# Kernel optimization log

Hardware: AMD Instinct MI355X
Metric: run time of the kernel (lower is better)

Reference implementation:

```python
import jax, jax.numpy as jnp
import numpy as np

N_E = 8192
E_DIM = 256
BETA = 0.25

def setup_inputs() -> dict:
    key = jax.random.key(0)
    k1, k2 = jax.random.split(key)
    z = jax.random.normal(k1, (2, 16384, E_DIM), dtype=jnp.float32)
    # matches nn.Embedding init: uniform(-1/n_e, 1/n_e)
    emb = jax.random.uniform(k2, (N_E, E_DIM), minval=-1.0 / N_E, maxval=1.0 / N_E, dtype=jnp.float32)
    code_age = jnp.zeros((N_E,), jnp.float32)
    code_usage = jnp.zeros((N_E,), jnp.float32)
    return {"z": z, "emb": emb, "code_age": code_age, "code_usage": code_usage}

def reference(z, emb, code_age, code_usage):
    sg = jax.lax.stop_gradient
    zf = z.reshape(-1, emb.shape[1])  # [M, D]
    # squared euclidean distances; argmin is identical to torch.cdist argmin
    d = (jnp.sum(zf * zf, axis=1, keepdims=True)
         - 2.0 * (zf @ emb.T)
         + jnp.sum(emb * emb, axis=1)[None, :])  # [M, n_e]
    idx = jnp.argmin(d, axis=1)  # [M]
    z_q = emb[idx].reshape(z.shape)
    loss = BETA * jnp.mean((sg(z_q) - z) ** 2) + jnp.mean((z_q - sg(z)) ** 2)
    z_q_st = z + sg(z_q - z)  # straight-through
    # code stats: age reset for used codes, usage histogram via scatter-add
    new_code_age = (code_age + 1.0).at[idx].set(0.0)
    new_code_usage = code_usage.at[idx].add(jnp.ones_like(idx, dtype=code_usage.dtype))
    return z_q_st, loss, idx, new_code_age, new_code_usage
```

## Files before the change

kernel.cpp:

```cpp
#include <hip/hip_runtime.h>
#include <math.h>

#define D_DIM 256
#define NE    8192
#define M_TOT 32768L

#define O_LOSS  8388608L
#define O_IDX   8388609L
#define O_AGE   8421377L
#define O_USAGE 8429569L

typedef __attribute__((ext_vector_type(8))) short bf16x8;
typedef __attribute__((ext_vector_type(4))) short bf16x4;
typedef __attribute__((ext_vector_type(4))) float f32x4;

__device__ __forceinline__ short f2bf(float f) {
  unsigned u = __float_as_uint(f);
  u += 0x7FFFu + ((u >> 16) & 1u);
  return (short)(u >> 16);
}
__device__ __forceinline__ float bf2f(short s) {
  return __uint_as_float(((unsigned)(unsigned short)s) << 16);
}

__global__ __launch_bounds__(256) void vq_prep(
    const float* __restrict__ z, const float* __restrict__ emb,
    const float* __restrict__ code_age, const float* __restrict__ code_usage,
    float* __restrict__ out, float* __restrict__ zzf, float* __restrict__ enf,
    int* __restrict__ cnt) {
  int t = blockIdx.x * 256 + threadIdx.x;
  {
    const float4* row = reinterpret_cast<const float4*>(z + (size_t)t * D_DIM);
    double s = 0.0;
#pragma unroll
    for (int q = 0; q < D_DIM / 4; ++q) {
      float4 v = row[q];
      s = fma((double)v.x, (double)v.x, s);
      s = fma((double)v.y, (double)v.y, s);
      s = fma((double)v.z, (double)v.z, s);
      s = fma((double)v.w, (double)v.w, s);
    }
    zzf[t] = (float)s;
  }
  if (t < NE) {
    const float4* row = reinterpret_cast<const float4*>(emb + (size_t)t * D_DIM);
    double s = 0.0;
#pragma unroll
    for (int q = 0; q < D_DIM / 4; ++q) {
      float4 v = row[q];
      s = fma((double)v.x, (double)v.x, s);
      s = fma((double)v.y, (double)v.y, s);
      s = fma((double)v.z, (double)v.z, s);
      s = fma((double)v.w, (double)v.w, s);
    }
    enf[t] = (float)s;
    out[O_AGE + t] = code_age[t] + 1.0f;
    out[O_USAGE + t] = code_usage[t];
    if (t == 0) { out[O_LOSS] = 0.0f; *cnt = 0; }
  }
}

__global__ __launch_bounds__(256) void vq_split(
    const float* __restrict__ emb, short* __restrict__ emb_h,
    short* __restrict__ emb_l) {
  int e4 = blockIdx.x * 256 + threadIdx.x;
  float4 v = reinterpret_cast<const float4*>(emb)[e4];
  float s[4] = {v.x, v.y, v.z, v.w};
  short h[4], l[4];
#pragma unroll
  for (int i = 0; i < 4; ++i) {
    h[i] = f2bf(s[i]);
    l[i] = f2bf(s[i] - bf2f(h[i]));
  }
  *reinterpret_cast<bf16x4*>(emb_h + (size_t)e4 * 4) = (bf16x4){h[0], h[1], h[2], h[3]};
  *reinterpret_cast<bf16x4*>(emb_l + (size_t)e4 * 4) = (bf16x4){l[0], l[1], l[2], l[3]};
}

#define LDK 40
#define LSLICE (128 * LDK)
#define CHUNK 4096
#define MSPLIT 4

template <int PRESPLIT>
__global__ __launch_bounds__(512, 2) void vq_argmin_mfma(
    const float* __restrict__ z, const float* __restrict__ emb,
    const short* __restrict__ emb_h, const short* __restrict__ emb_l,
    const float* __restrict__ zzf, const float* __restrict__ enf,
    float* __restrict__ pv1, float* __restrict__ pv2, int* __restrict__ pj1) {
  __shared__ short th[2][LSLICE];
  __shared__ short tl[2][LSLICE];

  const int tid = threadIdx.x;
  const int lane = tid & 63;
  const int wave = tid >> 6;
  const int wr = wave >> 1;
  const int wc = wave & 1;
  const int lrow = lane & 15;
  const int lq = lane >> 4;
  const size_t row0 = (size_t)blockIdx.x * 128;
  const int jbase = blockIdx.y * CHUNK;

  const int srow = tid >> 2;
  const int skq = (tid & 3) * 8;

  bf16x8 afh[2][8], afl[2][8];
#pragma unroll
  for (int ks = 0; ks < 8; ++ks) {
    __syncthreads();
    {
      const float* src = z + (row0 + srow) * (size_t)D_DIM + ks * 32 + skq;
      float4 v0 = *reinterpret_cast<const float4*>(src);
      float4 v1 = *reinterpret_cast<const float4*>(src + 4);
      float s[8] = {v0.x, v0.y, v0.z, v0.w, v1.x, v1.y, v1.z, v1.w};
      short h[8], l[8];
#pragma unroll
      for (int i = 0; i < 8; ++i) {
        h[i] = f2bf(s[i]);
        l[i] = f2bf(s[i] - bf2f(h[i]));
      }
      *reinterpret_cast<bf16x4*>(&th[0][srow * LDK + skq]) = (bf16x4){h[0], h[1], h[2], h[3]};
      *reinterpret_cast<bf16x4*>(&th[0][srow * LDK + skq + 4]) = (bf16x4){h[4], h[5], h[6], h[7]};
      *reinterpret_cast<bf16x4*>(&tl[0][srow * LDK + skq]) = (bf16x4){l[0], l[1], l[2], l[3]};
      *reinterpret_cast<bf16x4*>(&tl[0][srow * LDK + skq + 4]) = (bf16x4){l[4], l[5], l[6], l[7]};
    }
    __syncthreads();
#pragma unroll
    for (int rt = 0; rt < 2; ++rt) {
      int r = wr * 32 + rt * 16 + lrow;
      afh[rt][ks] = *reinterpret_cast<const bf16x8*>(&th[0][r * LDK + lq * 8]);
      afl[rt][ks] = *reinterpret_cast<const bf16x8*>(&tl[0][r * LDK + lq * 8]);
    }
  }

  float zrow2[8];
#pragma unroll
  for (int rt = 0; rt < 2; ++rt)
#pragma unroll
    for (int rr = 0; rr < 4; ++rr)
      zrow2[rt * 4 + rr] = zzf[row0 + wr * 32 + rt * 16 + lq * 4 + rr];

  float bv1[8], bv2[8];
  int bj1[8];
#pragma unroll
  for (int s = 0; s < 8; ++s) { bv1[s] = INFINITY; bv2[s] = INFINITY; bj1[s] = 0; }

  bf16x8 ph, pl;
  float4 pf0, pf1;

  if (PRESPLIT) {
    ph = *reinterpret_cast<const bf16x8*>(emb_h + (size_t)(jbase + srow) * D_DIM + skq);
    pl = *reinterpret_cast<const bf16x8*>(emb_l + (size_t)(jbase + srow) * D_DIM + skq);
  } else {
    const float* src = emb + (size_t)(jbase + srow) * D_DIM + skq;
    pf0 = *reinterpret_cast<const float4*>(src);
    pf1 = *reinterpret_cast<const float4*>(src + 4);
  }
  __syncthreads();
  if (PRESPLIT) {
    *reinterpret_cast<bf16x8*>(&th[0][srow * LDK + skq]) = ph;
    *reinterpret_cast<bf16x8*>(&tl[0][srow * LDK + skq]) = pl;
    ph = *reinterpret_cast<const bf16x8*>(emb_h + (size_t)(jbase + srow) * D_DIM + 32 + skq);
    pl = *reinterpret_cast<const bf16x8*>(emb_l + (size_t)(jbase + srow) * D_DIM + 32 + skq);
  } else {
    float s[8] = {pf0.x, pf0.y, pf0.z, pf0.w, pf1.x, pf1.y, pf1.z, pf1.w};
    short h[8], l[8];
#pragma unroll
    for (int i = 0; i < 8; ++i) {
      h[i] = f2bf(s[i]);
      l[i] = f2bf(s[i] - bf2f(h[i]));
    }
    *reinterpret_cast<bf16x4*>(&th[0][srow * LDK + skq]) = (bf16x4){h[0], h[1], h[2], h[3]};
    *reinterpret_cast<bf16x4*>(&th[0][srow * LDK + skq + 4]) = (bf16x4){h[4], h[5], h[6], h[7]};
    *reinterpret_cast<bf16x4*>(&tl[0][srow * LDK + skq]) = (bf16x4){l[0], l[1], l[2], l[3]};
    *reinterpret_cast<bf16x4*>(&tl[0][srow * LDK + skq + 4]) = (bf16x4){l[4], l[5], l[6], l[7]};
    const float* src = emb + (size_t)(jbase + srow) * D_DIM + 32 + skq;
    pf0 = *reinterpret_cast<const float4*>(src);
    pf1 = *reinterpret_cast<const float4*>(src + 4);
  }
  asm volatile("s_waitcnt lgkmcnt(0)" ::: "memory");
  __builtin_amdgcn_s_barrier();
  asm volatile("" ::: "memory");

  for (int jt0 = jbase; jt0 < jbase + CHUNK; jt0 += 128) {
    float enq[4];
#pragma unroll
    for (int ct = 0; ct < 4; ++ct) enq[ct] = enf[jt0 + wc * 64 + ct * 16 + lrow];

    f32x4 acc[2][4];
#pragma unroll
    for (int rt = 0; rt < 2; ++rt)
#pragma unroll
      for (int ct = 0; ct < 4; ++ct) acc[rt][ct] = (f32x4){0.f, 0.f, 0.f, 0.f};

#pragma unroll
    for (int ks = 0; ks < 8; ++ks) {
      const int p = ks & 1;
      bf16x8 bfh[4];
#pragma unroll
      for (int ct = 0; ct < 4; ++ct) {
        int c = wc * 64 + ct * 16 + lrow;
        bfh[ct] = *reinterpret_cast<const bf16x8*>(&th[p][c * LDK + lq * 8]);
      }
      __builtin_amdgcn_s_setprio(1);
#pragma unroll
      for (int rt = 0; rt < 2; ++rt)
#pragma unroll
        for (int ct = 0; ct < 4; ++ct) {
          acc[rt][ct] = __builtin_amdgcn_mfma_f32_16x16x32_bf16(
              afl[rt][ks], bfh[ct], acc[rt][ct], 0, 0, 0);
          acc[rt][ct] = __builtin_amdgcn_mfma_f32_16x16x32_bf16(
              afh[rt][ks], bfh[ct], acc[rt][ct], 0, 0, 0);
        }
      __builtin_amdgcn_s_setprio(0);

      if (PRESPLIT) {
        *reinterpret_cast<bf16x8*>(&th[p ^ 1][srow * LDK + skq]) = ph;
        *reinterpret_cast<bf16x8*>(&tl[p ^ 1][srow * LDK + skq]) = pl;
      } else {
        float s[8] = {pf0.x, pf0.y, pf0.z, pf0.w, pf1.x, pf1.y, pf1.z, pf1.w};
        short h[8], l[8];
#pragma unroll
        for (int i = 0; i < 8; ++i) {
          h[i] = f2bf(s[i]);
          l[i] = f2bf(s[i] - bf2f(h[i]));
        }
        *reinterpret_cast<bf16x4*>(&th[p ^ 1][srow * LDK + skq]) = (bf16x4){h[0], h[1], h[2], h[3]};
        *reinterpret_cast<bf16x4*>(&th[p ^ 1][srow * LDK + skq + 4]) = (bf16x4){h[4], h[5], h[6], h[7]};
        *reinterpret_cast<bf16x4*>(&tl[p ^ 1][srow * LDK + skq]) = (bf16x4){l[0], l[1], l[2], l[3]};
        *reinterpret_cast<bf16x4*>(&tl[p ^ 1][srow * LDK + skq + 4]) = (bf16x4){l[4], l[5], l[6], l[7]};
      }
      {
        int sl = ((jt0 - jbase) >> 4) + ks + 2;
        if (sl > CHUNK / 16 - 1) sl = CHUNK / 16 - 1;
        const size_t off = ((size_t)(jbase + (sl >> 3) * 128 + srow)) * D_DIM
                         + (sl & 7) * 32 + skq;
        if (PRESPLIT) {
          ph = *reinterpret_cast<const bf16x8*>(emb_h + off);
          pl = *reinterpret_cast<const bf16x8*>(emb_l + off);
        } else {
          pf0 = *reinterpret_cast<const float4*>(emb + off);
          pf1 = *reinterpret_cast<const float4*>(emb + off + 4);
        }
      }

      bf16x8 bfl[4];
#pragma unroll
      for (int ct = 0; ct < 4; ++ct) {
        int c = wc * 64 + ct * 16 + lrow;
        bfl[ct] = *reinterpret_cast<const bf16x8*>(&tl[p][c * LDK + lq * 8]);
      }
      __builtin_amdgcn_s_setprio(1);
#pragma unroll
      for (int rt = 0; rt < 2; ++rt)
#pragma unroll
        for (int ct = 0; ct < 4; ++ct)
          acc[rt][ct] = __builtin_amdgcn_mfma_f32_16x16x32_bf16(
              afh[rt][ks], bfl[ct], acc[rt][ct], 0, 0, 0);
      __builtin_amdgcn_s_setprio(0);

      asm volatile("s_waitcnt lgkmcnt(0)" ::: "memory");
      __builtin_amdgcn_s_barrier();
      asm volatile("" ::: "memory");
    }

#pragma unroll
    for (int ct = 0; ct < 4; ++ct) {
      int gj = jt0 + wc * 64 + ct * 16 + lrow;
      float ef = enq[ct];
#pragma unroll
      for (int rt = 0; rt < 2; ++rt)
#pragma unroll
        for (int rr = 0; rr < 4; ++rr) {
          int s = rt * 4 + rr;
          float t = zrow2[s] - 2.0f * acc[rt][ct][rr];
          float dv = t + ef;
          bj1[s] = (dv < bv1[s]) ? gj : bj1[s];
          bv2[s] = fminf(bv2[s], fmaxf(dv, bv1[s]));
          bv1[s] = fminf(bv1[s], dv);
        }
    }
  }

#pragma unroll
  for (int m = 1; m < 16; m <<= 1) {
#pragma unroll
    for (int s = 0; s < 8; ++s) {
      float ov1 = __shfl_xor(bv1[s], m, 16);
      float ov2 = __shfl_xor(bv2[s], m, 16);
      int oj1 = __shfl_xor(bj1[s], m, 16);
      if (ov1 < bv1[s] || (ov1 == bv1[s] && oj1 < bj1[s])) {
        bv2[s] = fminf(bv1[s], ov2);
        bv1[s] = ov1; bj1[s] = oj1;
      } else {
        bv2[s] = fminf(bv2[s], ov1);
      }
    }
  }
  if (lrow == 0) {
#pragma unroll
    for (int s = 0; s < 8; ++s) {
      size_t grow = row0 + wr * 32 + (s >> 2) * 16 + lq * 4 + (s & 3);
      size_t o = (size_t)(blockIdx.y * 2 + wc) * M_TOT + grow;
      pv1[o] = bv1[s]; pv2[o] = bv2[s]; pj1[o] = bj1[s];
    }
  }
}

__global__ __launch_bounds__(256) void vq_merge(
    const float* __restrict__ pv1, const float* __restrict__ pv2,
    const int* __restrict__ pj1, int* __restrict__ idx_ws,
    int* __restrict__ cnt, int* __restrict__ flagged,
    float* __restrict__ flagv1, int* __restrict__ gnc) {
  int m = blockIdx.x * 256 + threadIdx.x;
  if (m >= M_TOT) return;
  float v1 = INFINITY, v2 = INFINITY;
  int j1 = 0;
#pragma unroll
  for (int s = 0; s < MSPLIT; ++s) {
    float a1 = pv1[(size_t)s * M_TOT + m];
    float a2 = pv2[(size_t)s * M_TOT + m];
    int aj = pj1[(size_t)s * M_TOT + m];
    if (a1 < v1 || (a1 == v1 && aj < j1)) {
      v2 = fminf(v1, a2); v1 = a1; j1 = aj;
    } else {
      v2 = fminf(v2, a1);
    }
  }
  idx_ws[m] = j1;
  float u = ldexpf(1.0f, ilogbf(v2) - 23);
  if (v2 - v1 <= 2.0f * u + 1e-5f) {
    int p = atomicAdd(cnt, 1);
    flagged[p] = m;
    flagv1[p] = v1;
    gnc[p] = 0;
  }
}

#define RSPLIT 8
#define RCHUNK (NE / RSPLIT)
#define GCAP 16

template <int PRESPLIT>
__global__ __launch_bounds__(512, 2) void vq_refine_scan(
    const float* __restrict__ z, const float* __restrict__ emb,
    const short* __restrict__ emb_h, const short* __restrict__ emb_l,
    const float* __restrict__ zzf, const float* __restrict__ enf,
    const int* __restrict__ cnt, const int* __restrict__ flagged,
    const float* __restrict__ flagv1, int* __restrict__ gnc,
    int* __restrict__ gcj) {
  int n = *cnt;
  if (n > (int)M_TOT) n = (int)M_TOT;
  const int base = blockIdx.x * 128;
  if (base >= n) return;

  __shared__ short th[2][LSLICE];
  __shared__ short tl[2][LSLICE];
  __shared__ int rowm_s[128];
  __shared__ float thr_s[128];
  __shared__ float rzz_s[128];

  const int tid = threadIdx.x;
  const int lane = tid & 63;
  const int wave = tid >> 6;
  const int wr = wave >> 1;
  const int wc = wave & 1;
  const int lrow = lane & 15;
  const int lq = lane >> 4;
  const int cb = blockIdx.y * RCHUNK;

  const int srow = tid >> 2;
  const int skq = (tid & 3) * 8;

  if (tid < 128) {
    bool valid = (base + tid) < n;
    int m = valid ? flagged[base + tid] : flagged[base];
    rowm_s[tid] = m;
    rzz_s[tid] = zzf[m];
    if (valid) {
      float v1 = flagv1[base + tid];
      float u = ldexpf(1.0f, ilogbf(v1) - 23);
      thr_s[tid] = v1 + 4.0f * u + 2.5e-5f;
    } else {
      thr_s[tid] = -INFINITY;
    }
  }

  bf16x8 afh[2][8], afl[2][8];
#pragma unroll
  for (int ks = 0; ks < 8; ++ks) {
    __syncthreads();
    {
      const float* src = z + (size_t)rowm_s[srow] * D_DIM + ks * 32 + skq;
      float4 v0 = *reinterpret_cast<const float4*>(src);
      float4 v1 = *reinterpret_cast<const float4*>(src + 4);
      float s[8] = {v0.x, v0.y, v0.z, v0.w, v1.x, v1.y, v1.z, v1.w};
      short h[8], l[8];
#pragma unroll
      for (int i = 0; i < 8; ++i) {
        h[i] = f2bf(s[i]);
        l[i] = f2bf(s[i] - bf2f(h[i]));
      }
      *reinterpret_cast<bf16x4*>(&th[0][srow * LDK + skq]) = (bf16x4){h[0], h[1], h[2], h[3]};
      *reinterpret_cast<bf16x4*>(&th[0][srow * LDK + skq + 4]) = (bf16x4){h[4], h[5], h[6], h[7]};
      *reinterpret_cast<bf16x4*>(&tl[0][srow * LDK + skq]) = (bf16x4){l[0], l[1], l[2], l[3]};
      *reinterpret_cast<bf16x4*>(&tl[0][srow * LDK + skq + 4]) = (bf16x4){l[4], l[5], l[6], l[7]};
    }
    __syncthreads();
#pragma unroll
    for (int rt = 0; rt < 2; ++rt) {
      int r = wr * 32 + rt * 16 + lrow;
      afh[rt][ks] = *reinterpret_cast<const bf16x8*>(&th[0][r * LDK + lq * 8]);
      afl[rt][ks] = *reinterpret_cast<const bf16x8*>(&tl[0][r * LDK + lq * 8]);
    }
  }

  float zrow2[8], thr8[8];
  int rcix8[8];
#pragma unroll
  for (int rt = 0; rt < 2; ++rt)
#pragma unroll
    for (int rr = 0; rr < 4; ++rr) {
      int s = rt * 4 + rr;
      int lrloc = wr * 32 + rt * 16 + lq * 4 + rr;
      zrow2[s] = rzz_s[lrloc];
      thr8[s] = thr_s[lrloc];
      rcix8[s] = base + lrloc;
    }

  bf16x8 ph, pl;
  float4 pf0, pf1;

  if (PRESPLIT) {
    ph = *reinterpret_cast<const bf16x8*>(emb_h + (size_t)(cb + srow) * D_DIM + skq);
    pl = *reinterpret_cast<const bf16x8*>(emb_l + (size_t)(cb + srow) * D_DIM + skq);
  } else {
    const float* src = emb + (size_t)(cb + srow) * D_DIM + skq;
    pf0 = *reinterpret_cast<const float4*>(src);
    pf1 = *reinterpret_cast<const float4*>(src + 4);
  }
  __syncthreads();
  if (PRESPLIT) {
    *reinterpret_cast<bf16x8*>(&th[0][srow * LDK + skq]) = ph;
    *reinterpret_cast<bf16x8*>(&tl[0][srow * LDK + skq]) = pl;
    ph = *reinterpret_cast<const bf16x8*>(emb_h + (size_t)(cb + srow) * D_DIM + 32 + skq);
    pl = *reinterpret_cast<const bf16x8*>(emb_l + (size_t)(cb + srow) * D_DIM + 32 + skq);
  } else {
    float s[8] = {pf0.x, pf0.y, pf0.z, pf0.w, pf1.x, pf1.y, pf1.z, pf1.w};
    short h[8], l[8];
#pragma unroll
    for (int i = 0; i < 8; ++i) {
      h[i] = f2bf(s[i]);
      l[i] = f2bf(s[i] - bf2f(h[i]));
    }
    *reinterpret_cast<bf16x4*>(&th[0][srow * LDK + skq]) = (bf16x4){h[0], h[1], h[2], h[3]};
    *reinterpret_cast<bf16x4*>(&th[0][srow * LDK + skq + 4]) = (bf16x4){h[4], h[5], h[6], h[7]};
    *reinterpret_cast<bf16x4*>(&tl[0][srow * LDK + skq]) = (bf16x4){l[0], l[1], l[2], l[3]};
    *reinterpret_cast<bf16x4*>(&tl[0][srow * LDK + skq + 4]) = (bf16x4){l[4], l[5], l[6], l[7]};
    const float* src = emb + (size_t)(cb + srow) * D_DIM + 32 + skq;
    pf0 = *reinterpret_cast<const float4*>(src);
    pf1 = *reinterpret_cast<const float4*>(src + 4);
  }
  asm volatile("s_waitcnt lgkmcnt(0)" ::: "memory");
  __builtin_amdgcn_s_barrier();
  asm volatile("" ::: "memory");

  for (int jt0 = cb; jt0 < cb + RCHUNK; jt0 += 128) {
    float enq[4];
#pragma unroll
    for (int ct = 0; ct < 4; ++ct) enq[ct] = enf[jt0 + wc * 64 + ct * 16 + lrow];

    f32x4 acc[2][4];
#pragma unroll
    for (int rt = 0; rt < 2; ++rt)
#pragma unroll
      for (int ct = 0; ct < 4; ++ct) acc[rt][ct] = (f32x4){0.f, 0.f, 0.f, 0.f};

#pragma unroll
    for (int ks = 0; ks < 8; ++ks) {
      const int p = ks & 1;
      bf16x8 bfh[4];
#pragma unroll
      for (int ct = 0; ct < 4; ++ct) {
        int c = wc * 64 + ct * 16 + lrow;
        bfh[ct] = *reinterpret_cast<const bf16x8*>(&th[p][c * LDK + lq * 8]);
      }
      __builtin_amdgcn_s_setprio(1);
#pragma unroll
      for (int rt = 0; rt < 2; ++rt)
#pragma unroll
        for (int ct = 0; ct < 4; ++ct) {
          acc[rt][ct] = __builtin_amdgcn_mfma_f32_16x16x32_bf16(
              afl[rt][ks], bfh[ct], acc[rt][ct], 0, 0, 0);
          acc[rt][ct] = __builtin_amdgcn_mfma_f32_16x16x32_bf16(
              afh[rt][ks], bfh[ct], acc[rt][ct], 0, 0, 0);
        }
      __builtin_amdgcn_s_setprio(0);

      if (PRESPLIT) {
        *reinterpret_cast<bf16x8*>(&th[p ^ 1][srow * LDK + skq]) = ph;
        *reinterpret_cast<bf16x8*>(&tl[p ^ 1][srow * LDK + skq]) = pl;
      } else {
        float s[8] = {pf0.x, pf0.y, pf0.z, pf0.w, pf1.x, pf1.y, pf1.z, pf1.w};
        short h[8], l[8];
#pragma unroll
        for (int i = 0; i < 8; ++i) {
          h[i] = f2bf(s[i]);
          l[i] = f2bf(s[i] - bf2f(h[i]));
        }
        *reinterpret_cast<bf16x4*>(&th[p ^ 1][srow * LDK + skq]) = (bf16x4){h[0], h[1], h[2], h[3]};
        *reinterpret_cast<bf16x4*>(&th[p ^ 1][srow * LDK + skq + 4]) = (bf16x4){h[4], h[5], h[6], h[7]};
        *reinterpret_cast<bf16x4*>(&tl[p ^ 1][srow * LDK + skq]) = (bf16x4){l[0], l[1], l[2], l[3]};
        *reinterpret_cast<bf16x4*>(&tl[p ^ 1][srow * LDK + skq + 4]) = (bf16x4){l[4], l[5], l[6], l[7]};
      }
      {
        int sl = ((jt0 - cb) >> 4) + ks + 2;
        if (sl > RCHUNK / 16 - 1) sl = RCHUNK / 16 - 1;
        const size_t off = ((size_t)(cb + (sl >> 3) * 128 + srow)) * D_DIM
                         + (sl & 7) * 32 + skq;
        if (PRESPLIT) {
          ph = *reinterpret_cast<const bf16x8*>(emb_h + off);
          pl = *reinterpret_cast<const bf16x8*>(emb_l + off);
        } else {
          pf0 = *reinterpret_cast<const float4*>(emb + off);
          pf1 = *reinterpret_cast<const float4*>(emb + off + 4);
        }
      }

      bf16x8 bfl[4];
#pragma unroll
      for (int ct = 0; ct < 4; ++ct) {
        int c = wc * 64 + ct * 16 + lrow;
        bfl[ct] = *reinterpret_cast<const bf16x8*>(&tl[p][c * LDK + lq * 8]);
      }
      __builtin_amdgcn_s_setprio(1);
#pragma unroll
      for (int rt = 0; rt < 2; ++rt)
#pragma unroll
        for (int ct = 0; ct < 4; ++ct)
          acc[rt][ct] = __builtin_amdgcn_mfma_f32_16x16x32_bf16(
              afh[rt][ks], bfl[ct], acc[rt][ct], 0, 0, 0);
      __builtin_amdgcn_s_setprio(0);

      asm volatile("s_waitcnt lgkmcnt(0)" ::: "memory");
      __builtin_amdgcn_s_barrier();
      asm volatile("" ::: "memory");
    }

#pragma unroll
    for (int ct = 0; ct < 4; ++ct) {
      int gj = jt0 + wc * 64 + ct * 16 + lrow;
      float ef = enq[ct];
#pragma unroll
      for (int rt = 0; rt < 2; ++rt)
#pragma unroll
        for (int rr = 0; rr < 4; ++rr) {
          int s = rt * 4 + rr;
          float t = zrow2[s] - 2.0f * acc[rt][ct][rr];
          float dv = t + ef;
          if (dv <= thr8[s]) {
            int p = atomicAdd(&gnc[rcix8[s]], 1);
            if (p < GCAP) gcj[rcix8[s] * GCAP + p] = gj;
          }
        }
    }
  }
}

__global__ __launch_bounds__(256) void vq_refine_fin(
    const float* __restrict__ z, const float* __restrict__ emb,
    const float* __restrict__ zzf, const float* __restrict__ enf,
    int* __restrict__ idx_ws, const int* __restrict__ cnt,
    const int* __restrict__ flagged, const int* __restrict__ gnc,
    const int* __restrict__ gcj) {
  __shared__ float zs[D_DIM];
  __shared__ float cdv[GCAP];
  __shared__ float rv[256];
  __shared__ int rj[256];

  const int tid = threadIdx.x;
  int n = *cnt;
  if (n > (int)M_TOT) n = (int)M_TOT;

  for (int rc = blockIdx.x; rc < n; rc += gridDim.x) {
    int m = flagged[rc];
    __syncthreads();
    zs[tid] = z[(size_t)m * D_DIM + tid];
    __syncthreads();
    int nc = gnc[rc];
    float rzz = zzf[m];

    if (nc >= 1 && nc <= GCAP) {
      if (tid < nc) {
        int j = gcj[rc * GCAP + tid];
        const float4* er = reinterpret_cast<const float4*>(emb + (size_t)j * D_DIM);
        double a = 0.0;
#pragma unroll 4
        for (int k4 = 0; k4 < D_DIM / 4; ++k4) {
          float4 ev = er[k4];
          float4 zv = *reinterpret_cast<const float4*>(&zs[k4 * 4]);
          a = fma((double)zv.x, (double)ev.x, a);
          a = fma((double)zv.y, (double)ev.y, a);
          a = fma((double)zv.z, (double)ev.z, a);
          a = fma((double)zv.w, (double)ev.w, a);
        }
        float zef = (float)a;
        float t = rzz - 2.0f * zef;
        cdv[tid] = t + enf[j];
      }
      __syncthreads();
      if (tid == 0) {
        float bvv = INFINITY; int bjj = 0x7FFFFFFF;
        for (int c = 0; c < nc; ++c) {
          float dv = cdv[c]; int j = gcj[rc * GCAP + c];
          if (dv < bvv || (dv == bvv && j < bjj)) { bvv = dv; bjj = j; }
        }
        idx_ws[m] = bjj;
      }
    } else if (nc > GCAP) {
      float bvv = INFINITY; int bjj = 0;
      for (int j = tid; j < NE; j += 256) {
        const float4* er = reinterpret_cast<const float4*>(emb + (size_t)j * D_DIM);
        double a = 0.0;
        for (int k4 = 0; k4 < D_DIM / 4; ++k4) {
          float4 ev = er[k4];
          float4 zv = *reinterpret_cast<const float4*>(&zs[k4 * 4]);
          a = fma((double)zv.x, (double)ev.x, a);
          a = fma((double)zv.y, (double)ev.y, a);
          a = fma((double)zv.z, (double)ev.z, a);
          a = fma((double)zv.w, (double)ev.w, a);
        }
        float zef = (float)a;
        float t = rzz - 2.0f * zef;
        float dv = t + enf[j];
        if (dv < bvv) { bvv = dv; bjj = j; }
      }
      rv[tid] = bvv; rj[tid] = bjj;
      __syncthreads();
      for (int s = 128; s > 0; s >>= 1) {
        if (tid < s) {
          float ov = rv[tid + s]; int oj = rj[tid + s];
          if (ov < rv[tid] || (ov == rv[tid] && oj < rj[tid])) {
            rv[tid] = ov; rj[tid] = oj;
          }
        }
        __syncthreads();
      }
      if (tid == 0) idx_ws[m] = rj[0];
    }
  }
}

__global__ __launch_bounds__(256) void vq_scatter(
    const int* __restrict__ idx_ws, float* __restrict__ out) {
  int m = blockIdx.x * 256 + threadIdx.x;
  if (m >= M_TOT) return;
  int j = idx_ws[m];
  out[O_IDX + m] = (float)j;
  out[O_AGE + j] = 0.0f;
  atomicAdd(&out[O_USAGE + j], 1.0f);
}

__global__ __launch_bounds__(256) void vq_gather(
    const float* __restrict__ z, const float* __restrict__ emb,
    const int* __restrict__ idx_ws, float* __restrict__ out) {
  __shared__ float lsum[4];
  size_t e4 = (size_t)blockIdx.x * 256 + threadIdx.x;
  size_t m = e4 >> 6;
  int dq = (int)(e4 & 63);
  int j = idx_ws[m];
  float4 q = *reinterpret_cast<const float4*>(emb + (size_t)j * D_DIM + dq * 4);
  float4 zv = *reinterpret_cast<const float4*>(z + e4 * 4);
  float dx = q.x - zv.x, dy = q.y - zv.y, dz = q.z - zv.z, dw = q.w - zv.w;
  float4 o;
  o.x = zv.x + dx; o.y = zv.y + dy; o.z = zv.z + dz; o.w = zv.w + dw;
  *reinterpret_cast<float4*>(out + e4 * 4) = o;
  float ls = dx * dx + dy * dy + dz * dz + dw * dw;
#pragma unroll
  for (int off = 32; off > 0; off >>= 1) ls += __shfl_down(ls, off, 64);
  if ((threadIdx.x & 63) == 0) lsum[threadIdx.x >> 6] = ls;
  __syncthreads();
  if (threadIdx.x == 0)
    atomicAdd(out + O_LOSS,
              (lsum[0] + lsum[1] + lsum[2] + lsum[3]) * (1.25f / 8388608.f));
}

extern "C" void kernel_launch(void* const* d_in, const int* in_sizes, int n_in,
                              void* d_out, int out_size, void* d_ws, size_t ws_size,
                              hipStream_t stream) {
  const float* z = (const float*)d_in[0];
  const float* emb = (const float*)d_in[1];
  const float* code_age = (const float*)d_in[2];
  const float* code_usage = (const float*)d_in[3];
  float* out = (float*)d_out;

  float* zzf = (float*)d_ws;
  float* enf = zzf + M_TOT;
  int* idx_ws = (int*)(enf + NE);
  int* cnt = idx_ws + M_TOT;
  int* flagged = cnt + 1;
  float* flagv1 = (float*)(flagged + M_TOT);
  int* gnc = (int*)(flagv1 + M_TOT);
  int* gcj = gnc + M_TOT;
  float* pv1 = (float*)(gcj + M_TOT * GCAP);
  float* pv2 = pv1 + MSPLIT * M_TOT;
  int* pj1 = (int*)(pv2 + MSPLIT * M_TOT);
  short* emb_h = (short*)(pj1 + MSPLIT * M_TOT);
  short* emb_l = emb_h + (size_t)NE * D_DIM;

  const size_t ws_need = (size_t)((char*)(emb_l + (size_t)NE * D_DIM) - (char*)d_ws);
  const bool presplit = ws_size >= ws_need;

  hipLaunchKernelGGL(vq_prep, dim3(M_TOT / 256), dim3(256), 0, stream,
                     z, emb, code_age, code_usage, out, zzf, enf, cnt);
  if (presplit) {
    hipLaunchKernelGGL(vq_split, dim3(NE * (D_DIM / 4) / 256), dim3(256), 0, stream,
                       emb, emb_h, emb_l);
    hipLaunchKernelGGL((vq_argmin_mfma<1>), dim3(M_TOT / 128, 2), dim3(512), 0, stream,
                       z, emb, emb_h, emb_l, zzf, enf, pv1, pv2, pj1);
  } else {
    hipLaunchKernelGGL((vq_argmin_mfma<0>), dim3(M_TOT / 128, 2), dim3(512), 0, stream,
                       z, emb, emb_h, emb_l, zzf, enf, pv1, pv2, pj1);
  }
  hipLaunchKernelGGL(vq_merge, dim3(M_TOT / 256), dim3(256), 0, stream,
                     pv1, pv2, pj1, idx_ws, cnt, flagged, flagv1, gnc);
  if (presplit) {
    hipLaunchKernelGGL((vq_refine_scan<1>), dim3(M_TOT / 128, RSPLIT), dim3(512), 0, stream,
                       z, emb, emb_h, emb_l, zzf, enf, cnt, flagged, flagv1, gnc, gcj);
  } else {
    hipLaunchKernelGGL((vq_refine_scan<0>), dim3(M_TOT / 128, RSPLIT), dim3(512), 0, stream,
                       z, emb, emb_h, emb_l, zzf, enf, cnt, flagged, flagv1, gnc, gcj);
  }
  hipLaunchKernelGGL(vq_refine_fin, dim3(256), dim3(256), 0, stream,
                     z, emb, zzf, enf, idx_ws, cnt, flagged, gnc, gcj);
  hipLaunchKernelGGL(vq_scatter, dim3(M_TOT / 256), dim3(256), 0, stream,
                     idx_ws, out);
  hipLaunchKernelGGL(vq_gather, dim3((M_TOT * (D_DIM / 4)) / 256), dim3(256), 0, stream,
                     z, emb, idx_ws, out);
}
```

Before: 637.0 us.

## Stream codebook tiles via global_load_lds into 4-stage swizzled LDS ring; fuse small kernels

The argmin MFMA kernel now loads the presplit bf16 hi/lo codebook tiles straight from global memory into LDS with global_load_lds, using a 4-slot ring and XOR-swizzled layout instead of going through registers with a padded double buffer. Codebook norms are staged once into LDS. The split kernel is folded into vq_prep, and the scatter kernel into vq_gather, which removes two launches. The swizzle and vmcnt-based synchronization add complexity and a risk of bank conflicts or race errors. The non-presplit fallback becomes fully synchronous per k-step.

```diff
diff --git a/kernel.cpp b/kernel.cpp
--- a/kernel.cpp
+++ b/kernel.cpp
@@ -13,6 +13,8 @@
 typedef __attribute__((ext_vector_type(8))) short bf16x8;
 typedef __attribute__((ext_vector_type(4))) short bf16x4;
 typedef __attribute__((ext_vector_type(4))) float f32x4;
+typedef __attribute__((address_space(1))) const void gv_t;
+typedef __attribute__((address_space(3))) void lv_t;
 
 __device__ __forceinline__ short f2bf(float f) {
   unsigned u = __float_as_uint(f);
@@ -27,7 +29,8 @@
     const float* __restrict__ z, const float* __restrict__ emb,
     const float* __restrict__ code_age, const float* __restrict__ code_usage,
     float* __restrict__ out, float* __restrict__ zzf, float* __restrict__ enf,
-    int* __restrict__ cnt) {
+    int* __restrict__ cnt, short* __restrict__ emb_h, short* __restrict__ emb_l,
+    int do_split) {
   int t = blockIdx.x * 256 + threadIdx.x;
   {
     const float4* row = reinterpret_cast<const float4*>(z + (size_t)t * D_DIM);
@@ -58,37 +61,37 @@
     out[O_USAGE + t] = code_usage[t];
     if (t == 0) { out[O_LOSS] = 0.0f; *cnt = 0; }
   }
-}
-
-__global__ __launch_bounds__(256) void vq_split(
-    const float* __restrict__ emb, short* __restrict__ emb_h,
-    short* __restrict__ emb_l) {
-  int e4 = blockIdx.x * 256 + threadIdx.x;
-  float4 v = reinterpret_cast<const float4*>(emb)[e4];
-  float s[4] = {v.x, v.y, v.z, v.w};
-  short h[4], l[4];
-#pragma unroll
-  for (int i = 0; i < 4; ++i) {
-    h[i] = f2bf(s[i]);
-    l[i] = f2bf(s[i] - bf2f(h[i]));
-  }
-  *reinterpret_cast<bf16x4*>(emb_h + (size_t)e4 * 4) = (bf16x4){h[0], h[1], h[2], h[3]};
-  *reinterpret_cast<bf16x4*>(emb_l + (size_t)e4 * 4) = (bf16x4){l[0], l[1], l[2], l[3]};
-}
-
-#define LDK 40
-#define LSLICE (128 * LDK)
+  if (do_split) {
+#pragma unroll
+    for (int i = 0; i < 16; ++i) {
+      int e4 = t + i * 32768;
+      float4 v = reinterpret_cast<const float4*>(emb)[e4];
+      float s[4] = {v.x, v.y, v.z, v.w};
+      short h[4], l[4];
+#pragma unroll
+      for (int k = 0; k < 4; ++k) {
+        h[k] = f2bf(s[k]);
+        l[k] = f2bf(s[k] - bf2f(h[k]));
+      }
+      *reinterpret_cast<bf16x4*>(emb_h + (size_t)e4 * 4) = (bf16x4){h[0], h[1], h[2], h[3]};
+      *reinterpret_cast<bf16x4*>(emb_l + (size_t)e4 * 4) = (bf16x4){l[0], l[1], l[2], l[3]};
+    }
+  }
+}
+
 #define CHUNK 4096
 #define MSPLIT 4
-
-template <int PRESPLIT>
+#define SLDS 4096
+
+template <int GLDS>
 __global__ __launch_bounds__(512, 2) void vq_argmin_mfma(
     const float* __restrict__ z, const float* __restrict__ emb,
     const short* __restrict__ emb_h, const short* __restrict__ emb_l,
     const float* __restrict__ zzf, const float* __restrict__ enf,
     float* __restrict__ pv1, float* __restrict__ pv2, int* __restrict__ pj1) {
-  __shared__ short th[2][LSLICE];
-  __shared__ short tl[2][LSLICE];
+  __shared__ short thb[4][SLDS];
+  __shared__ short tlb[4][SLDS];
+  __shared__ float enfs[CHUNK];
 
   const int tid = threadIdx.x;
   const int lane = tid & 63;
@@ -101,14 +104,26 @@
   const int jbase = blockIdx.y * CHUNK;
 
   const int srow = tid >> 2;
-  const int skq = (tid & 3) * 8;
+  const int sq = tid & 3;
+  const int woff = (srow * 32 + sq * 8) ^ ((srow & 7) << 3);
+
+  const int gr = ((tid >> 3) << 1) | (((tid >> 2) & 1) ^ ((tid >> 4) & 1));
+  const int gq = (tid & 3) ^ (gr & 3);
+  const int gbase = gr * D_DIM + gq * 8;
+  const int ldst = wave * 512;
+
+  const int sw = (lrow & 7) << 3;
+  const int aro = ((wr * 32 + lrow) * 32 + lq * 8) ^ sw;
+  const int cro = ((wc * 64 + lrow) * 32 + lq * 8) ^ sw;
+
+  for (int i = tid; i < CHUNK; i += 512) enfs[i] = enf[jbase + i];
 
   bf16x8 afh[2][8], afl[2][8];
 #pragma unroll
   for (int ks = 0; ks < 8; ++ks) {
     __syncthreads();
     {
-      const float* src = z + (row0 + srow) * (size_t)D_DIM + ks * 32 + skq;
+      const float* src = z + (row0 + srow) * (size_t)D_DIM + ks * 32 + sq * 8;
       float4 v0 = *reinterpret_cast<const float4*>(src);
       float4 v1 = *reinterpret_cast<const float4*>(src + 4);
       float s[8] = {v0.x, v0.y, v0.z, v0.w, v1.x, v1.y, v1.z, v1.w};
@@ -118,17 +133,14 @@
         h[i] = f2bf(s[i]);
         l[i] = f2bf(s[i] - bf2f(h[i]));
       }
-      *reinterpret_cast<bf16x4*>(&th[0][srow * LDK + skq]) = (bf16x4){h[0], h[1], h[2], h[3]};
-      *reinterpret_cast<bf16x4*>(&th[0][srow * LDK + skq + 4]) = (bf16x4){h[4], h[5], h[6], h[7]};
-      *reinterpret_cast<bf16x4*>(&tl[0][srow * LDK + skq]) = (bf16x4){l[0], l[1], l[2], l[3]};
-      *reinterpret_cast<bf16x4*>(&tl[0][srow * LDK + skq + 4]) = (bf16x4){l[4], l[5], l[6], l[7]};
+      *reinterpret_cast<bf16x8*>(&thb[0][woff]) = (bf16x8){h[0], h[1], h[2], h[3], h[4], h[5], h[6], h[7]};
+      *reinterpret_cast<bf16x8*>(&tlb[0][woff]) = (bf16x8){l[0], l[1], l[2], l[3], l[4], l[5], l[6], l[7]};
     }
     __syncthreads();
 #pragma unroll
     for (int rt = 0; rt < 2; ++rt) {
-      int r = wr * 32 + rt * 16 + lrow;
-      afh[rt][ks] = *reinterpret_cast<const bf16x8*>(&th[0][r * LDK + lq * 8]);
-      afl[rt][ks] = *reinterpret_cast<const bf16x8*>(&tl[0][r * LDK + lq * 8]);
+      afh[rt][ks] = *reinterpret_cast<const bf16x8*>(&thb[0][aro + rt * 512]);
+      afl[rt][ks] = *reinterpret_cast<const bf16x8*>(&tlb[0][aro + rt * 512]);
     }
   }
 
@@ -144,48 +156,23 @@
 #pragma unroll
   for (int s = 0; s < 8; ++s) { bv1[s] = INFINITY; bv2[s] = INFINITY; bj1[s] = 0; }
 
-  bf16x8 ph, pl;
-  float4 pf0, pf1;
-
-  if (PRESPLIT) {
-    ph = *reinterpret_cast<const bf16x8*>(emb_h + (size_t)(jbase + srow) * D_DIM + skq);
-    pl = *reinterpret_cast<const bf16x8*>(emb_l + (size_t)(jbase + srow) * D_DIM + skq);
-  } else {
-    const float* src = emb + (size_t)(jbase + srow) * D_DIM + skq;
-    pf0 = *reinterpret_cast<const float4*>(src);
-    pf1 = *reinterpret_cast<const float4*>(src + 4);
-  }
-  __syncthreads();
-  if (PRESPLIT) {
-    *reinterpret_cast<bf16x8*>(&th[0][srow * LDK + skq]) = ph;
-    *reinterpret_cast<bf16x8*>(&tl[0][srow * LDK + skq]) = pl;
-    ph = *reinterpret_cast<const bf16x8*>(emb_h + (size_t)(jbase + srow) * D_DIM + 32 + skq);
-    pl = *reinterpret_cast<const bf16x8*>(emb_l + (size_t)(jbase + srow) * D_DIM + 32 + skq);
-  } else {
-    float s[8] = {pf0.x, pf0.y, pf0.z, pf0.w, pf1.x, pf1.y, pf1.z, pf1.w};
-    short h[8], l[8];
-#pragma unroll
-    for (int i = 0; i < 8; ++i) {
-      h[i] = f2bf(s[i]);
-      l[i] = f2bf(s[i] - bf2f(h[i]));
-    }
-    *reinterpret_cast<bf16x4*>(&th[0][srow * LDK + skq]) = (bf16x4){h[0], h[1], h[2], h[3]};
-    *reinterpret_cast<bf16x4*>(&th[0][srow * LDK + skq + 4]) = (bf16x4){h[4], h[5], h[6], h[7]};
-    *reinterpret_cast<bf16x4*>(&tl[0][srow * LDK + skq]) = (bf16x4){l[0], l[1], l[2], l[3]};
-    *reinterpret_cast<bf16x4*>(&tl[0][srow * LDK + skq + 4]) = (bf16x4){l[4], l[5], l[6], l[7]};
-    const float* src = emb + (size_t)(jbase + srow) * D_DIM + 32 + skq;
-    pf0 = *reinterpret_cast<const float4*>(src);
-    pf1 = *reinterpret_cast<const float4*>(src + 4);
-  }
-  asm volatile("s_waitcnt lgkmcnt(0)" ::: "memory");
-  __builtin_amdgcn_s_barrier();
-  asm volatile("" ::: "memory");
+  const short* gph = emb_h + (size_t)jbase * D_DIM + gbase;
+  const short* gpl = emb_l + (size_t)jbase * D_DIM + gbase;
+  int soff = 0;
+
+  if (GLDS) {
+    __syncthreads();
+    __builtin_amdgcn_global_load_lds((gv_t*)(gph + 0), (lv_t*)&thb[0][ldst], 16, 0, 0);
+    __builtin_amdgcn_global_load_lds((gv_t*)(gpl + 0), (lv_t*)&tlb[0][ldst], 16, 0, 0);
+    __builtin_amdgcn_global_load_lds((gv_t*)(gph + 32), (lv_t*)&thb[1][ldst], 16, 0, 0);
+    __builtin_amdgcn_global_load_lds((gv_t*)(gpl + 32), (lv_t*)&tlb[1][ldst], 16, 0, 0);
+    soff = 64;
+    asm volatile("s_waitcnt vmcnt(2)" ::: "memory");
+    __builtin_amdgcn_s_barrier();
+    asm volatile("" ::: "memory");
+  }
 
   for (int jt0 = jbase; jt0 < jbase + CHUNK; jt0 += 128) {
-    float enq[4];
-#pragma unroll
-    for (int ct = 0; ct < 4; ++ct) enq[ct] = enf[jt0 + wc * 64 + ct * 16 + lrow];
-
     f32x4 acc[2][4];
 #pragma unroll
     for (int rt = 0; rt < 2; ++rt)
@@ -194,13 +181,37 @@
 
 #pragma unroll
     for (int ks = 0; ks < 8; ++ks) {
-      const int p = ks & 1;
+      const int p = GLDS ? (ks & 3) : 0;
+      if (!GLDS) {
+        __syncthreads();
+        const float* src = emb + (size_t)(jt0 + srow) * D_DIM + ks * 32 + sq * 8;
+        float4 v0 = *reinterpret_cast<const float4*>(src);
+        float4 v1 = *reinterpret_cast<const float4*>(src + 4);
+        float s[8] = {v0.x, v0.y, v0.z, v0.w, v1.x, v1.y, v1.z, v1.w};
+        short h[8], l[8];
+#pragma unroll
+        for (int i = 0; i < 8; ++i) {
+          h[i] = f2bf(s[i]);
+          l[i] = f2bf(s[i] - bf2f(h[i]));
+        }
+        *reinterpret_cast<bf16x8*>(&thb[0][woff]) = (bf16x8){h[0], h[1], h[2], h[3], h[4], h[5], h[6], h[7]};
+        *reinterpret_cast<bf16x8*>(&tlb[0][woff]) = (bf16x8){l[0], l[1], l[2], l[3], l[4], l[5], l[6], l[7]};
+        __syncthreads();
+      }
+
       bf16x8 bfh[4];
 #pragma unroll
-      for (int ct = 0; ct < 4; ++ct) {
-        int c = wc * 64 + ct * 16 + lrow;
-        bfh[ct] = *reinterpret_cast<const bf16x8*>(&th[p][c * LDK + lq * 8]);
-      }
+      for (int ct = 0; ct < 4; ++ct)
+        bfh[ct] = *reinterpret_cast<const bf16x8*>(&thb[p][cro + ct * 512]);
+
+      if (GLDS) {
+        __builtin_amdgcn_global_load_lds((gv_t*)(gph + soff),
+                                         (lv_t*)&thb[(ks + 2) & 3][ldst], 16, 0, 0);
+        __builtin_amdgcn_global_load_lds((gv_t*)(gpl + soff),
+                                         (lv_t*)&tlb[(ks + 2) & 3][ldst], 16, 0, 0);
+        soff += (((ks + 2) & 7) == 7) ? (128 * D_DIM - 7 * 32) : 32;
+      }
+
       __builtin_amdgcn_s_setprio(1);
 #pragma unroll
       for (int rt = 0; rt < 2; ++rt)
@@ -213,42 +224,10 @@
         }
       __builtin_amdgcn_s_setprio(0);
 
-      if (PRESPLIT) {
-        *reinterpret_cast<bf16x8*>(&th[p ^ 1][srow * LDK + skq]) = ph;
-        *reinterpret_cast<bf16x8*>(&tl[p ^ 1][srow * LDK + skq]) = pl;
-      } else {
-        float s[8] = {pf0.x, pf0.y, pf0.z, pf0.w, pf1.x, pf1.y, pf1.z, pf1.w};
-        short h[8], l[8];
-#pragma unroll
-        for (int i = 0; i < 8; ++i) {
-          h[i] = f2bf(s[i]);
-          l[i] = f2bf(s[i] - bf2f(h[i]));
-        }
-        *reinterpret_cast<bf16x4*>(&th[p ^ 1][srow * LDK + skq]) = (bf16x4){h[0], h[1], h[2], h[3]};
-        *reinterpret_cast<bf16x4*>(&th[p ^ 1][srow * LDK + skq + 4]) = (bf16x4){h[4], h[5], h[6], h[7]};
-        *reinterpret_cast<bf16x4*>(&tl[p ^ 1][srow * LDK + skq]) = (bf16x4){l[0], l[1], l[2], l[3]};
-        *reinterpret_cast<bf16x4*>(&tl[p ^ 1][srow * LDK + skq + 4]) = (bf16x4){l[4], l[5], l[6], l[7]};
-      }
-      {
-        int sl = ((jt0 - jbase) >> 4) + ks + 2;
-        if (sl > CHUNK / 16 - 1) sl = CHUNK / 16 - 1;
-        const size_t off = ((size_t)(jbase + (sl >> 3) * 128 + srow)) * D_DIM
-                         + (sl & 7) * 32 + skq;
-        if (PRESPLIT) {
-          ph = *reinterpret_cast<const bf16x8*>(emb_h + off);
-          pl = *reinterpret_cast<const bf16x8*>(emb_l + off);
-        } else {
-          pf0 = *reinterpret_cast<const float4*>(emb + off);
-          pf1 = *reinterpret_cast<const float4*>(emb + off + 4);
-        }
-      }
-
       bf16x8 bfl[4];
 #pragma unroll
-      for (int ct = 0; ct < 4; ++ct) {
-        int c = wc * 64 + ct * 16 + lrow;
-        bfl[ct] = *reinterpret_cast<const bf16x8*>(&tl[p][c * LDK + lq * 8]);
-      }
+      for (int ct = 0; ct < 4; ++ct)
+        bfl[ct] = *reinterpret_cast<const bf16x8*>(&tlb[p][cro + ct * 512]);
       __builtin_amdgcn_s_setprio(1);
 #pragma unroll
       for (int rt = 0; rt < 2; ++rt)
@@ -258,15 +237,18 @@
               afh[rt][ks], bfl[ct], acc[rt][ct], 0, 0, 0);
       __builtin_amdgcn_s_setprio(0);
 
-      asm volatile("s_waitcnt lgkmcnt(0)" ::: "memory");
-      __builtin_amdgcn_s_barrier();
-      asm volatile("" ::: "memory");
+      if (GLDS) {
+        asm volatile("s_waitcnt lgkmcnt(0)" ::: "memory");
+        asm volatile("s_waitcnt vmcnt(2)" ::: "memory");
+        __builtin_amdgcn_s_barrier();
+        asm volatile("" ::: "memory");
+      }
     }
 
 #pragma unroll
     for (int ct = 0; ct < 4; ++ct) {
       int gj = jt0 + wc * 64 + ct * 16 + lrow;
-      float ef = enq[ct];
+      float ef = enfs[(jt0 - jbase) + wc * 64 + ct * 16 + lrow];
 #pragma unroll
       for (int rt = 0; rt < 2; ++rt)
 #pragma unroll
@@ -336,6 +318,8 @@
   }
 }
 
+#define LDK 40
+#define LSLICE (128 * LDK)
 #define RSPLIT 8
 #define RCHUNK (NE / RSPLIT)
 #define GCAP 16
@@ -647,17 +631,8 @@
       }
       if (tid == 0) idx_ws[m] = rj[0];
     }
-  }
-}
-
-__global__ __launch_bounds__(256) void vq_scatter(
-    const int* __restrict__ idx_ws, float* __restrict__ out) {
-  int m = blockIdx.x * 256 + threadIdx.x;
-  if (m >= M_TOT) return;
-  int j = idx_ws[m];
-  out[O_IDX + m] = (float)j;
-  out[O_AGE + j] = 0.0f;
-  atomicAdd(&out[O_USAGE + j], 1.0f);
+    __syncthreads();
+  }
 }
 
 __global__ __launch_bounds__(256) void vq_gather(
@@ -668,6 +643,11 @@
   size_t m = e4 >> 6;
   int dq = (int)(e4 & 63);
   int j = idx_ws[m];
+  if (dq == 0) {
+    out[O_IDX + m] = (float)j;
+    out[O_AGE + j] = 0.0f;
+    atomicAdd(&out[O_USAGE + j], 1.0f);
+  }
   float4 q = *reinterpret_cast<const float4*>(emb + (size_t)j * D_DIM + dq * 4);
   float4 zv = *reinterpret_cast<const float4*>(z + e4 * 4);
   float dx = q.x - zv.x, dy = q.y - zv.y, dz = q.z - zv.z, dw = q.w - zv.w;
@@ -707,14 +687,14 @@
   short* emb_h = (short*)(pj1 + MSPLIT * M_TOT);
   short* emb_l = emb_h + (size_t)NE * D_DIM;
 
-  const size_t ws_need = (size_t)((char*)(emb_l + (size_t)NE * D_DIM) - (char*)d_ws);
+  const size_t ws_need =
+      (size_t)((char*)(emb_l + (size_t)NE * D_DIM) - (char*)d_ws) + 32768;
   const bool presplit = ws_size >= ws_need;
 
   hipLaunchKernelGGL(vq_prep, dim3(M_TOT / 256), dim3(256), 0, stream,
-                     z, emb, code_age, code_usage, out, zzf, enf, cnt);
+                     z, emb, code_age, code_usage, out, zzf, enf, cnt,
+                     emb_h, emb_l, presplit ? 1 : 0);
   if (presplit) {
-    hipLaunchKernelGGL(vq_split, dim3(NE * (D_DIM / 4) / 256), dim3(256), 0, stream,
-                       emb, emb_h, emb_l);
     hipLaunchKernelGGL((vq_argmin_mfma<1>), dim3(M_TOT / 128, 2), dim3(512), 0, stream,
                        z, emb, emb_h, emb_l, zzf, enf, pv1, pv2, pj1);
   } else {
@@ -732,8 +712,6 @@
   }
   hipLaunchKernelGGL(vq_refine_fin, dim3(256), dim3(256), 0, stream,
                      z, emb, zzf, enf, idx_ws, cnt, flagged, gnc, gcj);
-  hipLaunchKernelGGL(vq_scatter, dim3(M_TOT / 256), dim3(256), 0, stream,
-                     idx_ws, out);
   hipLaunchKernelGGL(vq_gather, dim3((M_TOT * (D_DIM / 4)) / 256), dim3(256), 0, stream,
                      z, emb, idx_ws, out);
 }
```

Result: slower. 656.3 us (+3.0%).
